# Kernel tuning notes

Hardware: AMD Instinct MI355X
Metric: run time of the kernel (lower is better)

## Reference

```python
import jax, jax.numpy as jnp
import numpy as np

N = 50000      # nodes
E = 400000     # edges
H = 64         # hidden_dim
HEADS = 4
OUT = 64       # out_channels per head (concat=False -> mean over heads)
R = 4          # num_relations
EA = 16        # edge_attr_dim
REL = 8        # rel_emb_dim
ED = EA + REL  # GATv2 edge_dim
FFN = 128      # int(hidden_dim * ffn_ratio)
GRID = 5
ORDER = 3
K = GRID + ORDER          # 8 spline bases
GPTS = GRID + 2*ORDER + 1 # 12 extended grid points
EPS_LN = 1e-5


def make_grid(in_features):
    h_step = 2.0 / GRID  # grid_range (-1, 1)
    g = jnp.arange(-ORDER, GRID + ORDER + 1, dtype=jnp.float32) * h_step - 1.0
    return jnp.tile(g, (in_features, 1))  # [in, GPTS]


def setup_inputs() -> dict:
    key = jax.random.key(0)
    ks = jax.random.split(key, 24)
    s = 0.1
    inp = {
        "h": jax.random.normal(ks[0], (N, H), jnp.float32),
        "edge_index": jax.random.randint(ks[1], (2, E), 0, N, dtype=jnp.int64),
        "edge_attr": jax.random.normal(ks[2], (E, EA), jnp.float32),
        "edge_type": jax.random.randint(ks[3], (E,), 0, R, dtype=jnp.int64),
        # per-relation GATv2 parameters (stacked over relations)
        "rel_emb": jax.random.normal(ks[4], (R, REL), jnp.float32) * s,
        "rel_gate": jax.random.normal(ks[5], (R,), jnp.float32) * s,
        "Wl": jax.random.normal(ks[6], (R, H, HEADS*OUT), jnp.float32) * s,
        "bl": jnp.zeros((R, HEADS*OUT), jnp.float32),
        "Wr": jax.random.normal(ks[7], (R, H, HEADS*OUT), jnp.float32) * s,
        "br": jnp.zeros((R, HEADS*OUT), jnp.float32),
        "We": jax.random.normal(ks[8], (R, ED, HEADS*OUT), jnp.float32) * s,
        "be": jnp.zeros((R, HEADS*OUT), jnp.float32),
        "att": jax.random.normal(ks[9], (R, HEADS, OUT), jnp.float32) * s,
        "out_bias": jnp.zeros((R, OUT), jnp.float32),
        # LayerNorms
        "ln1_g": jnp.ones((H,), jnp.float32), "ln1_b": jnp.zeros((H,), jnp.float32),
        "ln2_g": jnp.ones((H,), jnp.float32), "ln2_b": jnp.zeros((H,), jnp.float32),
        # KAN layer 1: H -> FFN
        "base_w1": jax.random.normal(ks[10], (FFN, H), jnp.float32) * s,
        "spline_w1": jax.random.normal(ks[11], (FFN, H, K), jnp.float32) * s,
        "scaler1": 1.0 + jax.random.normal(ks[12], (FFN, H), jnp.float32) * s,
        "grid1": make_grid(H),
        # KAN layer 2: FFN -> H
        "base_w2": jax.random.normal(ks[13], (H, FFN), jnp.float32) * s,
        "spline_w2": jax.random.normal(ks[14], (H, FFN, K), jnp.float32) * s,
        "scaler2": 1.0 + jax.random.normal(ks[15], (H, FFN), jnp.float32) * s,
        "grid2": make_grid(FFN),
    }
    return inp


def b_splines(x, grid):
    # x: [n, in], grid: [in, GPTS] -> [n, in, K] (Cox-de Boor recursion)
    xe = x[..., None]
    b = ((xe >= grid[:, :-1]) & (xe < grid[:, 1:])).astype(x.dtype)
    for k in range(1, ORDER + 1):
        b = ((xe - grid[:, : -(k + 1)]) / (grid[:, k:-1] - grid[:, : -(k + 1)]) * b[..., :-1]
             + (grid[:, k + 1:] - xe) / (grid[:, k + 1:] - grid[:, 1:-k]) * b[..., 1:])
    return b


def kan_linear(x, base_w, spline_w, scaler, grid):
    base = jax.nn.silu(x) @ base_w.T
    sb = b_splines(x, grid)               # [n, in, K]
    sw = spline_w * scaler[..., None]     # [out, in, K]
    return base + jnp.einsum('nik,oik->no', sb, sw)


def layer_norm(x, g, b):
    mu = x.mean(-1, keepdims=True)
    var = ((x - mu) ** 2).mean(-1, keepdims=True)
    return (x - mu) * jax.lax.rsqrt(var + EPS_LN) * g + b


def gatv2_relation(h, src, dst, ea_full, mask, Wl, bl, Wr, br, We, be, att, ob):
    xl = (h @ Wl + bl).reshape(N, HEADS, OUT)   # lin_l(x) -> source transform
    xr = (h @ Wr + br).reshape(N, HEADS, OUT)   # lin_r(x) -> target transform
    e = (ea_full @ We + be).reshape(-1, HEADS, OUT)
    z = jax.nn.leaky_relu(xl[src] + xr[dst] + e, 0.2)   # [E, heads, out]
    logits = jnp.einsum('eho,ho->eh', z, att)
    neg = jnp.finfo(logits.dtype).min
    logits = jnp.where(mask[:, None], logits, neg)
    # segment softmax over destination nodes (only edges of this relation)
    m = jax.ops.segment_max(logits, dst, num_segments=N)
    ex = jnp.where(mask[:, None], jnp.exp(logits - m[dst]), 0.0)
    denom = jax.ops.segment_sum(ex, dst, num_segments=N) + 1e-16
    alpha = ex / denom[dst]                              # [E, heads]
    out = jax.ops.segment_sum(xl[src] * alpha[..., None], dst, num_segments=N)
    return out.mean(axis=1) + ob                          # concat=False -> head mean, + bias


def reference(h, edge_index, edge_attr, edge_type, rel_emb, rel_gate,
              Wl, bl, Wr, br, We, be, att, out_bias,
              ln1_g, ln1_b, ln2_g, ln2_b,
              base_w1, spline_w1, scaler1, grid1,
              base_w2, spline_w2, scaler2, grid2):
    src, dst = edge_index[0], edge_index[1]
    gate = jax.nn.softmax(rel_gate)  # all relations assumed active
    h_msg = jnp.zeros_like(h)
    for r in range(R):  # fixed small relation count
        mask = edge_type == r
        ea_full = jnp.concatenate(
            [edge_attr, jnp.broadcast_to(rel_emb[r], (E, REL))], axis=-1)
        h_r = gatv2_relation(h, src, dst, ea_full, mask,
                             Wl[r], bl[r], Wr[r], br[r], We[r], be[r],
                             att[r], out_bias[r])
        h_msg = h_msg + gate[r] * h_r
    x = layer_norm(h + h_msg, ln1_g, ln1_b)
    y = kan_linear(x, base_w1, spline_w1, scaler1, grid1)
    y = kan_linear(y, base_w2, spline_w2, scaler2, grid2)
    return layer_norm(x + y, ln2_g, ln2_b)
```

## Files before the change

kernel.cpp:

```cpp
#include <hip/hip_runtime.h>
#include <math.h>

#define DEV __device__ __forceinline__

constexpr int NN   = 50000;
constexpr int EE   = 400000;
constexpr int NB   = (EE + 255) / 256;

typedef short bf16x8 __attribute__((ext_vector_type(8)));
typedef float f32x4  __attribute__((ext_vector_type(4)));

DEV void atomicMaxF(float* addr, float val) {
    int iv = __float_as_int(val);
    if (iv >= 0) atomicMax((int*)addr, iv);
    else         atomicMin((unsigned int*)addr, __float_as_uint(val));
}

DEV float lrelu(float v) { return v >= 0.f ? v : 0.2f * v; }

DEV unsigned short f2bf(float f) {
    unsigned int u = __float_as_uint(f);
    u = (u + 0x7FFF + ((u >> 16) & 1)) >> 16;
    return (unsigned short)u;
}
DEV float bf2f(unsigned short u) {
    return __uint_as_float(((unsigned int)u) << 16);
}

__global__ void prep_small(const float* __restrict__ rel_gate,
                           const float* __restrict__ out_bias,
                           const float* __restrict__ rel_emb,
                           const float* __restrict__ We,
                           const float* __restrict__ be,
                           float* __restrict__ gate, float* __restrict__ biasvec,
                           float* __restrict__ ebase) {
    __shared__ float gs[4];
    int tid = threadIdx.x;
    if (tid == 0) {
        float g0 = rel_gate[0], g1 = rel_gate[1], g2 = rel_gate[2], g3 = rel_gate[3];
        float mx = fmaxf(fmaxf(g0, g1), fmaxf(g2, g3));
        float e0 = expf(g0 - mx), e1 = expf(g1 - mx), e2 = expf(g2 - mx), e3 = expf(g3 - mx);
        float s = e0 + e1 + e2 + e3;
        gs[0] = e0 / s; gs[1] = e1 / s; gs[2] = e2 / s; gs[3] = e3 / s;
        gate[0] = gs[0]; gate[1] = gs[1]; gate[2] = gs[2]; gate[3] = gs[3];
    }
    __syncthreads();
    if (tid < 64) {
        float b = 0.f;
        for (int r = 0; r < 4; ++r) b += gs[r] * out_bias[r * 64 + tid];
        biasvec[tid] = b;
    }
    for (int r = 0; r < 4; ++r) {
        float v = be[r * 256 + tid];
        for (int i = 0; i < 8; ++i)
            v += rel_emb[r * 8 + i] * We[((size_t)(r * 24 + 16 + i)) * 256 + tid];
        ebase[r * 256 + tid] = v;
    }
}

__global__ void prep_wpack(const float* __restrict__ bw1, const float* __restrict__ sw1,
                           const float* __restrict__ sc1,
                           const float* __restrict__ bw2, const float* __restrict__ sw2,
                           const float* __restrict__ sc2,
                           unsigned short* __restrict__ P1,
                           unsigned short* __restrict__ P2) {
    const int tot1 = 73728;
    const int tot  = tot1 + 73728;
    for (int idx = blockIdx.x * blockDim.x + threadIdx.x; idx < tot;
         idx += gridDim.x * blockDim.x) {
        bool l2 = idx >= tot1;
        int e = l2 ? idx - tot1 : idx;
        int i = e & 7, lane = (e >> 3) & 63, fi = e >> 9;
        int NF = l2 ? 4 : 8;
        int kb = fi / NF, fb = fi % NF;
        int k = kb * 32 + ((lane >> 4) << 3) + i;
        int f = fb * 16 + (lane & 15);
        float v;
        if (!l2) {
            if (k < 64) v = bw1[f * 64 + k];
            else { int t = k - 64; int ii = t >> 3, j = t & 7;
                   v = sw1[(f * 64 + ii) * 8 + j] * sc1[f * 64 + ii]; }
            P1[e] = f2bf(v);
        } else {
            if (k < 128) v = bw2[f * 128 + k];
            else { int t = k - 128; int ii = t >> 3, j = t & 7;
                   v = sw2[(f * 128 + ii) * 8 + j] * sc2[f * 128 + ii]; }
            P2[e] = f2bf(v);
        }
    }
}

__global__ void prep_wpack_lr(const float* __restrict__ Wl,
                              const float* __restrict__ Wr,
                              unsigned short* __restrict__ PLR) {
    int idx = blockIdx.x * blockDim.x + threadIdx.x;
    if (idx >= 4 * 32768) return;
    int r = idx >> 15, e = idx & 32767;
    int i = e & 7, lane = (e >> 3) & 63, fi = e >> 9;
    int kb = fi >> 5, fb = fi & 31;
    int k = kb * 32 + ((lane >> 4) << 3) + i;
    int f = fb * 16 + (lane & 15);
    float v = (f < 256) ? Wl[((size_t)(r * 64 + k)) * 256 + f]
                        : Wr[((size_t)(r * 64 + k)) * 256 + (f - 256)];
    PLR[idx] = f2bf(v);
}

__global__ void fill_init(float* __restrict__ hmsg, float* __restrict__ m,
                          float* __restrict__ den) {
    const int n1 = NN * 64, n2 = NN * 16;
    const int tot = n1 + n2 + n2;
    for (int i = blockIdx.x * blockDim.x + threadIdx.x; i < tot;
         i += gridDim.x * blockDim.x) {
        if (i < n1) hmsg[i] = 0.f;
        else if (i < n1 + n2) m[i - n1] = -3.402823466e38f;
        else den[i - n1 - n2] = 0.f;
    }
}

__global__ void count_hist(const int* __restrict__ etype, int* __restrict__ bc) {
    __shared__ int lc[4];
    int tid = threadIdx.x;
    if (tid < 4) lc[tid] = 0;
    __syncthreads();
    int e = blockIdx.x * 256 + tid;
    if (e < EE) atomicAdd(&lc[etype[e]], 1);
    __syncthreads();
    if (tid < 4) bc[blockIdx.x * 4 + tid] = lc[tid];
}

__global__ void scan_blocks(const int* __restrict__ bc, int* __restrict__ bbase,
                            int* __restrict__ cnt) {
    int w = threadIdx.x >> 6, lane = threadIdx.x & 63;
    int running = 0;
    for (int b0 = 0; b0 < NB; b0 += 64) {
        int b = b0 + lane;
        int v = (b < NB) ? bc[b * 4 + w] : 0;
        int s = v;
#pragma unroll
        for (int off = 1; off < 64; off <<= 1) {
            int t = __shfl_up(s, off, 64);
            if (lane >= off) s += t;
        }
        if (b < NB) bbase[b * 4 + w] = running + s - v;
        running += __shfl(s, 63, 64);
    }
    if (lane == 0) cnt[w] = running;
}

__global__ void scatter_kernel(const int* __restrict__ etype,
                               const int* __restrict__ bbase,
                               int* __restrict__ eids) {
    __shared__ int lbase[4], lofs[4];
    int tid = threadIdx.x;
    if (tid < 4) { lbase[tid] = bbase[blockIdx.x * 4 + tid]; lofs[tid] = 0; }
    __syncthreads();
    int e = blockIdx.x * 256 + tid;
    if (e < EE) {
        int t = etype[e];
        int p = atomicAdd(&lofs[t], 1);
        eids[t * EE + lbase[t] + p] = e;
    }
}

__global__ __launch_bounds__(256) void gemm_mfma_xlxr(
    const float* __restrict__ hin, const unsigned short* __restrict__ P,
    const float* __restrict__ bl, const float* __restrict__ br,
    unsigned short* __restrict__ XLb, unsigned short* __restrict__ XRb) {
    int tid = threadIdx.x, wv = tid >> 6, lane = tid & 63;
    int row0 = blockIdx.x * 32;
    f32x4 acc[2][8];
#pragma unroll
    for (int rf = 0; rf < 2; ++rf)
#pragma unroll
        for (int cf = 0; cf < 8; ++cf) acc[rf][cf] = (f32x4){0.f, 0.f, 0.f, 0.f};
#pragma unroll
    for (int kb = 0; kb < 2; ++kb) {
        bf16x8 a[2];
#pragma unroll
        for (int rf = 0; rf < 2; ++rf) {
            int row = row0 + rf * 16 + (lane & 15);
            int k0 = kb * 32 + ((lane >> 4) << 3);
            bf16x8 av = (bf16x8){0, 0, 0, 0, 0, 0, 0, 0};
            if (row < NN) {
                const float4 f0 = *reinterpret_cast<const float4*>(
                    hin + (size_t)row * 64 + k0);
                const float4 f1 = *reinterpret_cast<const float4*>(
                    hin + (size_t)row * 64 + k0 + 4);
                av[0] = (short)f2bf(f0.x); av[1] = (short)f2bf(f0.y);
                av[2] = (short)f2bf(f0.z); av[3] = (short)f2bf(f0.w);
                av[4] = (short)f2bf(f1.x); av[5] = (short)f2bf(f1.y);
                av[6] = (short)f2bf(f1.z); av[7] = (short)f2bf(f1.w);
            }
            a[rf] = av;
        }
#pragma unroll
        for (int cf = 0; cf < 8; ++cf) {
            int fi = kb * 32 + wv * 8 + cf;
            bf16x8 b = *(const bf16x8*)(P + (((size_t)fi * 64 + lane) << 3));
            acc[0][cf] = __builtin_amdgcn_mfma_f32_16x16x32_bf16(a[0], b, acc[0][cf], 0, 0, 0);
            acc[1][cf] = __builtin_amdgcn_mfma_f32_16x16x32_bf16(a[1], b, acc[1][cf], 0, 0, 0);
        }
    }
#pragma unroll
    for (int cf = 0; cf < 8; ++cf) {
        int fc = (wv * 8 + cf) * 16 + (lane & 15);
        bool left = fc < 256;
        float bias = left ? bl[fc] : br[fc - 256];
        unsigned short* base = left ? (XLb + fc) : (XRb + (fc - 256));
#pragma unroll
        for (int rf = 0; rf < 2; ++rf)
#pragma unroll
            for (int r4 = 0; r4 < 4; ++r4) {
                int grow = row0 + rf * 16 + ((lane >> 4) << 2) + r4;
                if (grow < NN)
                    base[(size_t)grow * 256] = f2bf(acc[rf][cf][r4] + bias);
            }
    }
}

__global__ void pass1_kernel(const int* __restrict__ eidx, const float* __restrict__ eattr,
                             const int* __restrict__ eids, const int* __restrict__ cnt, int r,
                             const float* __restrict__ We, const float* __restrict__ att,
                             const float* __restrict__ ebase,
                             const unsigned short* __restrict__ XLb,
                             const unsigned short* __restrict__ XRb,
                             float* __restrict__ elog, float* __restrict__ mbuf) {
    __shared__ float4 we_s[16 * 64];
    __shared__ float4 att_s[64];
    __shared__ float4 eb_s[64];
    int tid = threadIdx.x;
    for (int i = tid; i < 16 * 256; i += 256) {
        int k = i >> 8, j = i & 255;
        ((float*)we_s)[i] = We[((size_t)(r * 24 + k)) * 256 + j];
    }
    ((float*)att_s)[tid] = att[r * 256 + tid];
    ((float*)eb_s)[tid]  = ebase[r * 256 + tid];
    __syncthreads();
    int cntr = cnt[r];
    int wave = (blockIdx.x << 2) + (tid >> 6);
    int lane = tid & 63;
    int nw = gridDim.x << 2;
    for (int i = wave; i < cntr; i += nw) {
        int e = eids[r * EE + i];
        int src = eidx[e], dst = eidx[EE + e];
        float ea[16];
#pragma unroll
        for (int k = 0; k < 16; ++k) ea[k] = eattr[(size_t)e * 16 + k];
        const ushort4 xlu = *reinterpret_cast<const ushort4*>(
            XLb + (size_t)src * 256 + lane * 4);
        const ushort4 xru = *reinterpret_cast<const ushort4*>(
            XRb + (size_t)dst * 256 + lane * 4);
        float4 ev = eb_s[lane];
#pragma unroll
        for (int k = 0; k < 16; ++k) {
            float4 w = we_s[k * 64 + lane];
            ev.x = fmaf(ea[k], w.x, ev.x);
            ev.y = fmaf(ea[k], w.y, ev.y);
            ev.z = fmaf(ea[k], w.z, ev.z);
            ev.w = fmaf(ea[k], w.w, ev.w);
        }
        float4 z;
        z.x = lrelu(bf2f(xlu.x) + bf2f(xru.x) + ev.x);
        z.y = lrelu(bf2f(xlu.y) + bf2f(xru.y) + ev.y);
        z.z = lrelu(bf2f(xlu.z) + bf2f(xru.z) + ev.z);
        z.w = lrelu(bf2f(xlu.w) + bf2f(xru.w) + ev.w);
        float4 a4 = att_s[lane];
        float p = z.x * a4.x + z.y * a4.y + z.z * a4.z + z.w * a4.w;
        p += __shfl_xor(p, 1, 64);
        p += __shfl_xor(p, 2, 64);
        p += __shfl_xor(p, 4, 64);
        p += __shfl_xor(p, 8, 64);
        if ((lane & 15) == 0) {
            int hh = lane >> 4;
            elog[(size_t)e * 4 + hh] = p;
            atomicMaxF(mbuf + ((size_t)r * NN + dst) * 4 + hh, p);
        }
    }
}

__global__ void pass2_kernel(const int* __restrict__ eidx, const int* __restrict__ eids,
                             const int* __restrict__ cnt, int r,
                             float* __restrict__ elog, const float* __restrict__ mbuf,
                             float* __restrict__ den) {
    int cntr = cnt[r];
    int tot = cntr * 4;
    for (int idx = blockIdx.x * blockDim.x + threadIdx.x; idx < tot;
         idx += gridDim.x * blockDim.x) {
        int i = idx >> 2, hh = idx & 3;
        int e = eids[r * EE + i];
        int dst = eidx[EE + e];
        size_t mi = ((size_t)r * NN + dst) * 4 + hh;
        float ex = expf(elog[(size_t)e * 4 + hh] - mbuf[mi]);
        elog[(size_t)e * 4 + hh] = ex;
        atomicAdd(den + mi, ex);
    }
}

__global__ void pass3_kernel(const int* __restrict__ eidx, const int* __restrict__ eids,
                             const int* __restrict__ cnt, int r,
                             const float* __restrict__ elog, const float* __restrict__ den,
                             const float* __restrict__ gate,
                             const unsigned short* __restrict__ XLb,
                             float* __restrict__ hmsg) {
    int cntr = cnt[r];
    float coef = 0.25f * gate[r];
    int wave = (blockIdx.x << 2) + (threadIdx.x >> 6);
    int lane = threadIdx.x & 63;
    int nw = gridDim.x << 2;
    for (int i = wave; i < cntr; i += nw) {
        int e = eids[r * EE + i];
        int src = eidx[e], dst = eidx[EE + e];
        size_t mb = ((size_t)r * NN + dst) * 4;
        float a0 = elog[(size_t)e * 4 + 0] / (den[mb + 0] + 1e-16f);
        float a1 = elog[(size_t)e * 4 + 1] / (den[mb + 1] + 1e-16f);
        float a2 = elog[(size_t)e * 4 + 2] / (den[mb + 2] + 1e-16f);
        float a3 = elog[(size_t)e * 4 + 3] / (den[mb + 3] + 1e-16f);
        const unsigned short* xlp = XLb + (size_t)src * 256;
        float val = a0 * bf2f(xlp[lane]) + a1 * bf2f(xlp[64 + lane]) +
                    a2 * bf2f(xlp[128 + lane]) + a3 * bf2f(xlp[192 + lane]);
        atomicAdd(hmsg + (size_t)dst * 64 + lane, coef * val);
    }
}

__global__ void ln_kernel(const float* __restrict__ a, const float* __restrict__ badd,
                          const float* __restrict__ biasvec,
                          const float* __restrict__ g, const float* __restrict__ b,
                          float* __restrict__ out) {
    int row = blockIdx.x * 4 + (threadIdx.x >> 6);
    int l = threadIdx.x & 63;
    if (row >= NN) return;
    float v = a[(size_t)row * 64 + l] + badd[(size_t)row * 64 + l];
    if (biasvec) v += biasvec[l];
    float s = v;
#pragma unroll
    for (int mm = 1; mm < 64; mm <<= 1) s += __shfl_xor(s, mm, 64);
    float mu = s * (1.f / 64.f);
    float d = v - mu;
    float s2 = d * d;
#pragma unroll
    for (int mm = 1; mm < 64; mm <<= 1) s2 += __shfl_xor(s2, mm, 64);
    float var = s2 * (1.f / 64.f);
    out[(size_t)row * 64 + l] = d * rsqrtf(var + 1e-5f) * g[l] + b[l];
}

template <int IN, int F, int NWF, int NCH>
__global__ __launch_bounds__(256) void kan_mfma(const float* __restrict__ Xin,
                                                const unsigned short* __restrict__ P,
                                                const float* __restrict__ grid,
                                                float* __restrict__ Yout) {
    constexpr int ICH = IN / NCH;
    constexpr int KC  = ICH * 9;
    constexpr int RS  = KC * 2;
    constexpr int NF  = F / 16;
    constexpr int SKB = ICH / 32;
    constexpr int PKB = ICH * 8 / 32;
    __shared__ __align__(16) unsigned short act[32 * KC];
    __shared__ float gp[2];
    int tid = threadIdx.x;
    if (tid == 0) {
        float g0 = grid[0];
        gp[0] = g0;
        gp[1] = 1.f / (grid[1] - g0);
    }
    __syncthreads();
    float g0 = gp[0], invh = gp[1];
    int row0 = blockIdx.x * 32;
    int wv = tid >> 6, lane = tid & 63;
    f32x4 acc[2][NWF];
#pragma unroll
    for (int rf = 0; rf < 2; ++rf)
#pragma unroll
        for (int cf = 0; cf < NWF; ++cf) acc[rf][cf] = (f32x4){0.f, 0.f, 0.f, 0.f};

    for (int c = 0; c < NCH; ++c) {
        if (c > 0) __syncthreads();
        constexpr int PER = 32 * ICH / 256;
#pragma unroll
        for (int p = 0; p < PER; ++p) {
            int flat = p * 256 + tid;
            int row = flat / ICH, i = flat % ICH;
            int n = row0 + row;
            float x = (n < NN) ? Xin[(size_t)n * IN + c * ICH + i] : 0.f;
            float sig = 1.f / (1.f + expf(-x));
            char* rowp = (char*)act + row * RS;
            unsigned int sw = (unsigned int)(row & 7) << 4;
            *(unsigned short*)(rowp + ((i * 2) ^ sw)) = f2bf(x * sig);
            int sb = (ICH + i * 8) * 2;
            *(uint4*)(rowp + (sb ^ sw)) = (uint4){0u, 0u, 0u, 0u};
            float pos = (x - g0) * invh;
            float jf = floorf(pos);
            int j = (int)jf;
            float u = pos - jf;
            if (j >= 0 && j <= 10) {
                float u2 = u * u, u3 = u2 * u;
                float om = 1.f - u;
                const float s6 = 1.f / 6.f;
                float v0 = u3 * s6;
                float v1 = (-3.f * u3 + 3.f * u2 + 3.f * u + 1.f) * s6;
                float v2 = (3.f * u3 - 6.f * u2 + 4.f) * s6;
                float v3 = om * om * om * s6;
                if (j < 8)
                    *(unsigned short*)(rowp + ((sb + j * 2) ^ sw)) = f2bf(v0);
                if (j >= 1 && j <= 8)
                    *(unsigned short*)(rowp + ((sb + (j - 1) * 2) ^ sw)) = f2bf(v1);
                if (j >= 2 && j <= 9)
                    *(unsigned short*)(rowp + ((sb + (j - 2) * 2) ^ sw)) = f2bf(v2);
                if (j >= 3)
                    *(unsigned short*)(rowp + ((sb + (j - 3) * 2) ^ sw)) = f2bf(v3);
            }
        }
        __syncthreads();
        constexpr int KBC = KC / 32;
        for (int kbl = 0; kbl < KBC; ++kbl) {
            int gkb = (kbl < SKB) ? (c * SKB + kbl)
                                  : (IN / 32 + c * PKB + (kbl - SKB));
            bf16x8 a[2];
#pragma unroll
            for (int rf = 0; rf < 2; ++rf) {
                int row = rf * 16 + (lane & 15);
                int o = (kbl * 64 + ((lane >> 4) * 16)) ^ ((row & 7) << 4);
                a[rf] = *(const bf16x8*)((char*)act + row * RS + o);
            }
#pragma unroll
            for (int cf = 0; cf < NWF; ++cf) {
                int fi = gkb * NF + wv * NWF + cf;
                bf16x8 b = *(const bf16x8*)(P + (((size_t)fi * 64 + lane) << 3));
#pragma unroll
                for (int rf = 0; rf < 2; ++rf)
                    acc[rf][cf] = __builtin_amdgcn_mfma_f32_16x16x32_bf16(
                        a[rf], b, acc[rf][cf], 0, 0, 0);
            }
        }
    }
#pragma unroll
    for (int rf = 0; rf < 2; ++rf)
#pragma unroll
        for (int cf = 0; cf < NWF; ++cf)
#pragma unroll
            for (int r4 = 0; r4 < 4; ++r4) {
                int grow = row0 + rf * 16 + ((lane >> 4) * 4) + r4;
                int f = (wv * NWF + cf) * 16 + (lane & 15);
                if (grow < NN) Yout[(size_t)grow * F + f] = acc[rf][cf][r4];
            }
}

extern "C" void kernel_launch(void* const* d_in, const int* in_sizes, int n_in,
                              void* d_out, int out_size, void* d_ws, size_t ws_size,
                              hipStream_t stream) {
    const float* h        = (const float*)d_in[0];
    const int*   eidx     = (const int*)d_in[1];
    const float* eattr    = (const float*)d_in[2];
    const int*   etype    = (const int*)d_in[3];
    const float* rel_emb  = (const float*)d_in[4];
    const float* rel_gate = (const float*)d_in[5];
    const float* Wl       = (const float*)d_in[6];
    const float* bl       = (const float*)d_in[7];
    const float* Wr       = (const float*)d_in[8];
    const float* br       = (const float*)d_in[9];
    const float* We       = (const float*)d_in[10];
    const float* be       = (const float*)d_in[11];
    const float* att      = (const float*)d_in[12];
    const float* out_bias = (const float*)d_in[13];
    const float* ln1_g    = (const float*)d_in[14];
    const float* ln1_b    = (const float*)d_in[15];
    const float* ln2_g    = (const float*)d_in[16];
    const float* ln2_b    = (const float*)d_in[17];
    const float* bw1      = (const float*)d_in[18];
    const float* sw1      = (const float*)d_in[19];
    const float* sc1      = (const float*)d_in[20];
    const float* grid1    = (const float*)d_in[21];
    const float* bw2      = (const float*)d_in[22];
    const float* sw2      = (const float*)d_in[23];
    const float* sc2      = (const float*)d_in[24];
    const float* grid2    = (const float*)d_in[25];
    float* out = (float*)d_out;
    float* W = (float*)d_ws;

    unsigned short* XLb = (unsigned short*)(W + 0);
    unsigned short* XRb = (unsigned short*)(W + 12800000);
    float* HM    = W + 25600000;
    float* M     = W + 28800000;
    float* DENb  = W + 29600000;
    float* EL    = W + 30400000;
    int*   EIDS  = (int*)(W + 32000000);
    int*   CNT   = (int*)(W + 33600000);
    float* GATE  = W + 33600064;
    float* BIAS  = W + 33600128;
    float* EBASE = W + 33600192;
    unsigned short* P1  = (unsigned short*)(W + 33601216);
    unsigned short* P2  = (unsigned short*)(W + 33638080);
    unsigned short* PLR = (unsigned short*)(W + 33674944);
    float* X  = W + 0;
    float* Y1 = W + 3200000;
    float* Y2 = W + 9600000;
    int* BC = (int*)(W + 12800000);
    int* BB = (int*)(W + 12800000 + 8192);

    prep_small<<<1, 256, 0, stream>>>(rel_gate, out_bias, rel_emb, We, be,
                                      GATE, BIAS, EBASE);
    prep_wpack<<<576, 256, 0, stream>>>(bw1, sw1, sc1, bw2, sw2, sc2, P1, P2);
    prep_wpack_lr<<<512, 256, 0, stream>>>(Wl, Wr, PLR);
    fill_init<<<2048, 256, 0, stream>>>(HM, M, DENb);
    count_hist<<<NB, 256, 0, stream>>>(etype, BC);
    scan_blocks<<<1, 256, 0, stream>>>(BC, BB, CNT);
    scatter_kernel<<<NB, 256, 0, stream>>>(etype, BB, EIDS);

    for (int r = 0; r < 4; ++r) {
        gemm_mfma_xlxr<<<(NN + 31) / 32, 256, 0, stream>>>(
            h, PLR + (size_t)r * 32768, bl + r * 256, br + r * 256, XLb, XRb);
        pass1_kernel<<<1024, 256, 0, stream>>>(eidx, eattr, EIDS, CNT, r, We, att,
                                               EBASE, XLb, XRb, EL, M);
        pass2_kernel<<<1024, 256, 0, stream>>>(eidx, EIDS, CNT, r, EL, M, DENb);
        pass3_kernel<<<1024, 256, 0, stream>>>(eidx, EIDS, CNT, r, EL, DENb, GATE,
                                               XLb, HM);
    }

    ln_kernel<<<(NN + 3) / 4, 256, 0, stream>>>(h, HM, BIAS, ln1_g, ln1_b, X);
    kan_mfma<64, 128, 2, 1><<<(NN + 31) / 32, 256, 0, stream>>>(X, P1, grid1, Y1);
    kan_mfma<128, 64, 1, 2><<<(NN + 31) / 32, 256, 0, stream>>>(Y1, P2, grid2, Y2);
    ln_kernel<<<(NN + 3) / 4, 256, 0, stream>>>(X, Y2, nullptr, ln2_g, ln2_b, out);
}
```

Measured before the change: 694.9 us.

## Build KAN MFMA operands directly in registers instead of LDS staging

The KAN layers now compute SiLU and B-spline basis values straight into MFMA A-fragment registers per lane. This removes the shared-memory staging buffer and the block barriers. In exchange, each of the four waves recomputes the same activations and spline bases redundantly. Every 16-row fragment also rereads the input from global memory, which adds more ALU work and more global loads.

```diff
diff --git a/kernel.cpp b/kernel.cpp
--- a/kernel.cpp
+++ b/kernel.cpp
@@ -343,55 +343,72 @@
     out[(size_t)row * 64 + l] = d * rsqrtf(var + 1e-5f) * g[l] + b[l];
 }
 
-template <int IN, int F, int NWF, int NCH>
-__global__ __launch_bounds__(256) void kan_mfma(const float* __restrict__ Xin,
-                                                const unsigned short* __restrict__ P,
-                                                const float* __restrict__ grid,
-                                                float* __restrict__ Yout) {
-    constexpr int ICH = IN / NCH;
-    constexpr int KC  = ICH * 9;
-    constexpr int RS  = KC * 2;
+template <int IN, int F, int NWF>
+__global__ __launch_bounds__(256) void kan_mfma_reg(const float* __restrict__ Xin,
+                                                    const unsigned short* __restrict__ P,
+                                                    const float* __restrict__ grid,
+                                                    float* __restrict__ Yout) {
+    constexpr int KB  = IN * 9 / 32;
+    constexpr int SKB = IN / 32;
     constexpr int NF  = F / 16;
-    constexpr int SKB = ICH / 32;
-    constexpr int PKB = ICH * 8 / 32;
-    __shared__ __align__(16) unsigned short act[32 * KC];
-    __shared__ float gp[2];
+    float g0 = grid[0];
+    float invh = 1.f / (grid[1] - g0);
     int tid = threadIdx.x;
-    if (tid == 0) {
-        float g0 = grid[0];
-        gp[0] = g0;
-        gp[1] = 1.f / (grid[1] - g0);
-    }
-    __syncthreads();
-    float g0 = gp[0], invh = gp[1];
+    int wv = tid >> 6, lane = tid & 63;
     int row0 = blockIdx.x * 32;
-    int wv = tid >> 6, lane = tid & 63;
+    int hi = lane >> 4;
     f32x4 acc[2][NWF];
 #pragma unroll
     for (int rf = 0; rf < 2; ++rf)
 #pragma unroll
         for (int cf = 0; cf < NWF; ++cf) acc[rf][cf] = (f32x4){0.f, 0.f, 0.f, 0.f};
 
-    for (int c = 0; c < NCH; ++c) {
-        if (c > 0) __syncthreads();
-        constexpr int PER = 32 * ICH / 256;
-#pragma unroll
-        for (int p = 0; p < PER; ++p) {
-            int flat = p * 256 + tid;
-            int row = flat / ICH, i = flat % ICH;
-            int n = row0 + row;
-            float x = (n < NN) ? Xin[(size_t)n * IN + c * ICH + i] : 0.f;
-            float sig = 1.f / (1.f + expf(-x));
-            char* rowp = (char*)act + row * RS;
-            unsigned int sw = (unsigned int)(row & 7) << 4;
-            *(unsigned short*)(rowp + ((i * 2) ^ sw)) = f2bf(x * sig);
-            int sb = (ICH + i * 8) * 2;
-            *(uint4*)(rowp + (sb ^ sw)) = (uint4){0u, 0u, 0u, 0u};
-            float pos = (x - g0) * invh;
-            float jf = floorf(pos);
-            int j = (int)jf;
-            float u = pos - jf;
-            if (j >= 0 && j <= 10) {
+#pragma unroll
+    for (int kb = 0; kb < SKB; ++kb) {
+        bf16x8 a[2];
+#pragma unroll
+        for (int rf = 0; rf < 2; ++rf) {
+            int row = row0 + rf * 16 + (lane & 15);
+            int k0 = kb * 32 + (hi << 3);
+            bf16x8 av = (bf16x8){0, 0, 0, 0, 0, 0, 0, 0};
+            if (row < NN) {
+                const float4 f0 = *reinterpret_cast<const float4*>(
+                    Xin + (size_t)row * IN + k0);
+                const float4 f1 = *reinterpret_cast<const float4*>(
+                    Xin + (size_t)row * IN + k0 + 4);
+                float xs[8] = {f0.x, f0.y, f0.z, f0.w, f1.x, f1.y, f1.z, f1.w};
+#pragma unroll
+                for (int i = 0; i < 8; ++i) {
+                    float x = xs[i];
+                    av[i] = (short)f2bf(x / (1.f + expf(-x)));
+                }
+            }
+            a[rf] = av;
+        }
+#pragma unroll
+        for (int cf = 0; cf < NWF; ++cf) {
+            int fi = kb * NF + wv * NWF + cf;
+            bf16x8 b = *(const bf16x8*)(P + (((size_t)fi * 64 + lane) << 3));
+#pragma unroll
+            for (int rf = 0; rf < 2; ++rf)
+                acc[rf][cf] = __builtin_amdgcn_mfma_f32_16x16x32_bf16(
+                    a[rf], b, acc[rf][cf], 0, 0, 0);
+        }
+    }
+#pragma unroll
+    for (int kb = SKB; kb < KB; ++kb) {
+        bf16x8 a[2];
+#pragma unroll
+        for (int rf = 0; rf < 2; ++rf) {
+            int row = row0 + rf * 16 + (lane & 15);
+            int ii = (kb - SKB) * 4 + hi;
+            bf16x8 av = (bf16x8){0, 0, 0, 0, 0, 0, 0, 0};
+            if (row < NN) {
+                float x = Xin[(size_t)row * IN + ii];
+                float pos = (x - g0) * invh;
+                float jf = floorf(pos);
+                int j = (int)jf;
+                float u = pos - jf;
                 float u2 = u * u, u3 = u2 * u;
                 float om = 1.f - u;
                 const float s6 = 1.f / 6.f;
@@ -399,37 +416,26 @@
                 float v1 = (-3.f * u3 + 3.f * u2 + 3.f * u + 1.f) * s6;
                 float v2 = (3.f * u3 - 6.f * u2 + 4.f) * s6;
                 float v3 = om * om * om * s6;
-                if (j < 8)
-                    *(unsigned short*)(rowp + ((sb + j * 2) ^ sw)) = f2bf(v0);
-                if (j >= 1 && j <= 8)
-                    *(unsigned short*)(rowp + ((sb + (j - 1) * 2) ^ sw)) = f2bf(v1);
-                if (j >= 2 && j <= 9)
-                    *(unsigned short*)(rowp + ((sb + (j - 2) * 2) ^ sw)) = f2bf(v2);
-                if (j >= 3)
-                    *(unsigned short*)(rowp + ((sb + (j - 3) * 2) ^ sw)) = f2bf(v3);
+                bool ok = (j >= 0) && (j <= 10);
+#pragma unroll
+                for (int s = 0; s < 8; ++s) {
+                    float vs = (j == s) ? v0 :
+                               (j == s + 1) ? v1 :
+                               (j == s + 2) ? v2 :
+                               (j == s + 3) ? v3 : 0.f;
+                    av[s] = ok ? (short)f2bf(vs) : (short)0;
+                }
             }
-        }
-        __syncthreads();
-        constexpr int KBC = KC / 32;
-        for (int kbl = 0; kbl < KBC; ++kbl) {
-            int gkb = (kbl < SKB) ? (c * SKB + kbl)
-                                  : (IN / 32 + c * PKB + (kbl - SKB));
-            bf16x8 a[2];
-#pragma unroll
-            for (int rf = 0; rf < 2; ++rf) {
-                int row = rf * 16 + (lane & 15);
-                int o = (kbl * 64 + ((lane >> 4) * 16)) ^ ((row & 7) << 4);
-                a[rf] = *(const bf16x8*)((char*)act + row * RS + o);
-            }
-#pragma unroll
-            for (int cf = 0; cf < NWF; ++cf) {
-                int fi = gkb * NF + wv * NWF + cf;
-                bf16x8 b = *(const bf16x8*)(P + (((size_t)fi * 64 + lane) << 3));
-#pragma unroll
-                for (int rf = 0; rf < 2; ++rf)
-                    acc[rf][cf] = __builtin_amdgcn_mfma_f32_16x16x32_bf16(
-                        a[rf], b, acc[rf][cf], 0, 0, 0);
-            }
+            a[rf] = av;
+        }
+#pragma unroll
+        for (int cf = 0; cf < NWF; ++cf) {
+            int fi = kb * NF + wv * NWF + cf;
+            bf16x8 b = *(const bf16x8*)(P + (((size_t)fi * 64 + lane) << 3));
+#pragma unroll
+            for (int rf = 0; rf < 2; ++rf)
+                acc[rf][cf] = __builtin_amdgcn_mfma_f32_16x16x32_bf16(
+                    a[rf], b, acc[rf][cf], 0, 0, 0);
         }
     }
 #pragma unroll
@@ -516,7 +522,7 @@
     }
 
     ln_kernel<<<(NN + 3) / 4, 256, 0, stream>>>(h, HM, BIAS, ln1_g, ln1_b, X);
-    kan_mfma<64, 128, 2, 1><<<(NN + 31) / 32, 256, 0, stream>>>(X, P1, grid1, Y1);
-    kan_mfma<128, 64, 1, 2><<<(NN + 31) / 32, 256, 0, stream>>>(Y1, P2, grid2, Y2);
+    kan_mfma_reg<64, 128, 2><<<(NN + 31) / 32, 256, 0, stream>>>(X, P1, grid1, Y1);
+    kan_mfma_reg<128, 64, 1><<<(NN + 31) / 32, 256, 0, stream>>>(Y1, P2, grid2, Y2);
     ln_kernel<<<(NN + 3) / 4, 256, 0, stream>>>(X, Y2, nullptr, ln2_g, ln2_b, out);
 }
```

After: 881.8 us. 1.27x slower.
